# Performance work log

Hardware: AMD Instinct MI355X
Metric: run time of the kernel (lower is better)

Reference implementation:

```python
import jax, jax.numpy as jnp
import numpy as np

# geomloss SamplesLoss defaults: loss='sinkhorn', p=2, blur=0.05, scaling=0.5,
# reach=None (balanced -> dampening lambda = 1), diameter=3, debias=False.
P = 2
DIAMETER = 3.0
BLUR = 0.05
SCALING = 0.5
MARGIN = 0.1
GAMMA = 10.0
# geomloss epsilon_schedule(p, diameter, blur, scaling)
EPS_LIST = [DIAMETER ** P] \
    + [float(np.exp(e)) for e in np.arange(P * np.log(DIAMETER), P * np.log(BLUR), P * np.log(SCALING))] \
    + [BLUR ** P]
NEG_INF_LOGW = -100000.0  # geomloss log_weights() sentinel for zero weights


def similarity_cost(xa, xb, gamma=GAMMA):
    # F.normalize(x, dim=-1): x / max(||x||, 1e-12)
    xa = xa / jnp.clip(jnp.linalg.norm(xa, axis=-1, keepdims=True), 1e-12)
    xb = xb / jnp.clip(jnp.linalg.norm(xb, axis=-1, keepdims=True), 1e-12)
    sim = jnp.exp(jnp.einsum('bnd,bmd->bnm', xa, xb) * gamma)  # (B, N, M)
    sim_c = sim.sum(axis=1, keepdims=True)  # column sums (B, 1, M)
    sim_r = sim.sum(axis=2, keepdims=True)  # row sums    (B, N, 1)
    return 1.0 - sim / (sim_c + sim_r - sim)


def softmin(eps, C, h):
    # geomloss softmin_tensorized: -eps * logsumexp_j(h_j - C_ij/eps)
    # C: (B, N, M), h: (B_or_1, M) -> (B, N)
    return -eps * jax.nn.logsumexp(h[:, None, :] - C / eps, axis=2)


def sinkhorn_ot(alpha, a_log, beta, b_log, f1, f2):
    # geomloss sinkhorn_tensorized with debias=False, balanced OT.
    C_xy = similarity_cost(f1, jax.lax.stop_gradient(f2))  # cost(x, y.detach())
    C_yx = similarity_cost(f2, jax.lax.stop_gradient(f1))  # cost(y, x.detach())
    C_xy_sg = jax.lax.stop_gradient(C_xy)
    C_yx_sg = jax.lax.stop_gradient(C_yx)

    eps = EPS_LIST[0]
    g_ab = softmin(eps, C_yx_sg, a_log)  # dual potential on y
    f_ba = softmin(eps, C_xy_sg, b_log)  # dual potential on x
    for eps in EPS_LIST:
        # symmetric (averaged) Sinkhorn updates, no grad (geomloss runs under no_grad)
        ft = softmin(eps, C_xy_sg, b_log + g_ab / eps)
        gt = softmin(eps, C_yx_sg, a_log + f_ba / eps)
        f_ba, g_ab = 0.5 * (f_ba + ft), 0.5 * (g_ab + gt)

    # last extrapolation: only differentiable step (detached dual inputs)
    eps = EPS_LIST[-1]
    f_ba_new = softmin(eps, C_xy, jax.lax.stop_gradient(b_log + g_ab / eps))
    g_ab_new = softmin(eps, C_yx, jax.lax.stop_gradient(a_log + f_ba / eps))

    # sinkhorn_cost (debias=False): <alpha, f_ba> + <beta, g_ab>
    return (alpha * f_ba_new).sum(axis=1) + (beta * g_ab_new).sum(axis=1)  # (B,)


def setup_inputs() -> dict:
    key = jax.random.key(0)
    k1, k2, k3, k4, k5 = jax.random.split(key, 5)
    B, N, N1, M1, D = 16, 512, 384, 384, 256
    return {
        'x1': jax.random.normal(k1, (B, N, D), dtype=jnp.float32),
        'x2': jax.random.normal(k2, (B, N, D), dtype=jnp.float32),
        'x3': jax.random.normal(k3, (B, N1, D), dtype=jnp.float32),
        'x4': jax.random.normal(k4, (B, M1, D), dtype=jnp.float32),
        'dist': jax.random.normal(k5, (16,), dtype=jnp.float32),  # stored but unused
    }


def reference(x1, x2, x3, x4, dist):
    B, N, _ = x1.shape
    N1 = x3.shape[1]
    M1 = x4.shape[1]
    dt = x1.dtype
    # marginals: ones over real points, zeros over padding points
    alpha = jnp.concatenate([jnp.ones((1, N), dt), jnp.zeros((1, N1), dt)], axis=1)
    beta = jnp.concatenate([jnp.ones((1, N), dt), jnp.zeros((1, M1), dt)], axis=1)
    a_log = jnp.concatenate([jnp.zeros((1, N), dt), jnp.full((1, N1), NEG_INF_LOGW, dt)], axis=1)
    b_log = jnp.concatenate([jnp.zeros((1, N), dt), jnp.full((1, M1), NEG_INF_LOGW, dt)], axis=1)

    f1 = jnp.concatenate([x1, x3], axis=1)  # (B, N+N1, D)
    f2 = jnp.concatenate([x2, x4], axis=1)  # (B, N+M1, D)

    ot_loss = sinkhorn_ot(alpha, a_log, beta, b_log, f1, f2)  # (B,)
    scon_cost = jnp.mean(ot_loss)[None]  # sum(ot_loss)/B, shape (1,)

    hinge = jax.nn.relu(MARGIN - jnp.einsum('bnd,bmd->bnm', x3, x4)).sum()
    hinge_cost = hinge[None]  # shape (1,)

    # original returns {'hinge_cost': ..., 'scon_cost': ...}; pack as (2,) array
    return jnp.concatenate([hinge_cost, scon_cost])
```

## Files before the change

### kernel.cpp

```cpp
#include <hip/hip_runtime.h>
#include <cstddef>
#include <cstdint>

#define BATCH 16
#define NFULL 896
#define NREAL 512
#define NPAD  384
#define DIM   256

typedef short bf16x8 __attribute__((ext_vector_type(8)));
typedef short s16x4  __attribute__((ext_vector_type(4)));
typedef float f32x4  __attribute__((ext_vector_type(4)));
typedef int   int4v  __attribute__((ext_vector_type(4)));

static __device__ inline short f2bf(float v) {
    unsigned u = __float_as_uint(v);
    unsigned r = (u + 0x7FFFu + ((u >> 16) & 1u)) >> 16;
    return (short)r;
}
static __device__ inline float bf2f(short s) {
    return __uint_as_float(((unsigned)(unsigned short)s) << 16);
}

__global__ __launch_bounds__(256) void norm_cvt_kernel(
    const float* __restrict__ x1, const float* __restrict__ x3,
    const float* __restrict__ x2, const float* __restrict__ x4,
    short* __restrict__ A1s, short* __restrict__ B2s,
    float* __restrict__ invn1, float* __restrict__ invn2,
    float* __restrict__ n1, float* __restrict__ n2,
    float* __restrict__ zero_base, float* __restrict__ out)
{
    const int t = threadIdx.x;
    const int gid = blockIdx.x * 256 + t;
    if (gid < 2 * BATCH * NFULL) zero_base[gid] = 0.f;
    if (gid < 2) out[gid] = 0.f;

    const int w = t >> 6, lane = t & 63;
    const int rg = blockIdx.x * 4 + w;
    const int side = rg >= BATCH * NFULL;
    const int rem  = rg - (side ? BATCH * NFULL : 0);
    const int b = rem / NFULL, row = rem % NFULL;
    const float* src;
    if (!side) src = (row < NREAL) ? x1 + ((size_t)b * NREAL + row) * DIM
                                   : x3 + ((size_t)b * NPAD + (row - NREAL)) * DIM;
    else       src = (row < NREAL) ? x2 + ((size_t)b * NREAL + row) * DIM
                                   : x4 + ((size_t)b * NPAD + (row - NREAL)) * DIM;
    const f32x4 v = ((const f32x4*)src)[lane];
    float ss = v[0]*v[0] + v[1]*v[1] + v[2]*v[2] + v[3]*v[3];
    #pragma unroll
    for (int m = 1; m < 64; m <<= 1) ss += __shfl_xor(ss, m);
    const float nrm = sqrtf(ss);
    const float inv = 1.0f / fmaxf(nrm, 1e-12f);
    if (lane == 0) {
        (side ? invn2 : invn1)[b * NFULL + row] = inv;
        (side ? n2 : n1)[b * NFULL + row] = nrm;
    }
    s16x4 hi, lo;
    #pragma unroll
    for (int c = 0; c < 4; ++c) {
        const float val = v[c] * inv;
        hi[c] = f2bf(val);
        lo[c] = f2bf(val - bf2f(hi[c]));
    }
    short* dst = (side ? B2s : A1s) + ((size_t)b * NFULL + row) * 512;
    *(s16x4*)(dst + lane * 4) = hi;
    *(s16x4*)(dst + 256 + lane * 4) = lo;
}

__global__ __launch_bounds__(256) void gram_mfma_kernel(
    const short* __restrict__ A1s, const short* __restrict__ B2s,
    const float* __restrict__ n1, const float* __restrict__ n2,
    float* __restrict__ S, float* __restrict__ rowsum, float* __restrict__ colsum,
    float* __restrict__ out_hinge)
{
    const int flat = blockIdx.x;
    const int id = (flat & 7) * 98 + (flat >> 3);
    const int b  = id / 49;
    const int r49 = id % 49;
    const int by = r49 / 7, bx = r49 % 7;
    const int i0 = by * 128;
    const int j0 = bx * 128;
    __shared__ __align__(16) short As[128][72];
    __shared__ __align__(16) short Bs[128][72];
    const int t = threadIdx.x;
    const int wid = t >> 6, lane = t & 63;
    const int wr = wid >> 1, wc = wid & 1;
    const int lr = lane & 15, lg = lane >> 4;
    f32x4 acc[4][4] = {};

    const short* gA = A1s + ((size_t)b * NFULL + i0) * 512;
    const short* gB = B2s + ((size_t)b * NFULL + j0) * 512;

    for (int step = 0; step < 12; ++step) {
        const int kb   = step * 64;
        const int koff = kb & 255;
        const int aoff = (((kb >> 8) == 1) ? 256 : 0) + koff;
        const int boff = (((kb >> 8) == 2) ? 256 : 0) + koff;
        __syncthreads();
        #pragma unroll
        for (int p = 0; p < 4; ++p) {
            const int s = p * 256 + t;
            const int row = s >> 3, c = s & 7;
            *(int4v*)((char*)&As[0][0] + row * 144 + c * 16) =
                *(const int4v*)(gA + (size_t)row * 512 + aoff + c * 8);
            *(int4v*)((char*)&Bs[0][0] + row * 144 + c * 16) =
                *(const int4v*)(gB + (size_t)row * 512 + boff + c * 8);
        }
        __syncthreads();
        #pragma unroll
        for (int kk = 0; kk < 64; kk += 32) {
            bf16x8 af[4], bg[4];
            #pragma unroll
            for (int m = 0; m < 4; ++m)
                af[m] = *(const bf16x8*)((const char*)&As[0][0]
                         + (wr * 64 + m * 16 + lr) * 144 + kk * 2 + lg * 16);
            #pragma unroll
            for (int n = 0; n < 4; ++n)
                bg[n] = *(const bf16x8*)((const char*)&Bs[0][0]
                         + (wc * 64 + n * 16 + lr) * 144 + kk * 2 + lg * 16);
            #pragma unroll
            for (int m = 0; m < 4; ++m)
                #pragma unroll
                for (int n = 0; n < 4; ++n)
                    acc[m][n] = __builtin_amdgcn_mfma_f32_16x16x32_bf16(
                        af[m], bg[n], acc[m][n], 0, 0, 0);
        }
    }

    const bool storeS = (by < 4) && (bx < 4);
    const bool hingeB = (by >= 4) && (bx >= 4);
    float rp[4][4] = {};
    float cp[4] = {};
    float hp = 0.f;
    #pragma unroll
    for (int m = 0; m < 4; ++m) {
        const int row0 = i0 + wr * 64 + m * 16 + lg * 4;
        float n1v[4] = {0.f, 0.f, 0.f, 0.f};
        if (hingeB) {
            #pragma unroll
            for (int r = 0; r < 4; ++r) n1v[r] = n1[b * NFULL + row0 + r];
        }
        #pragma unroll
        for (int n = 0; n < 4; ++n) {
            const int col = j0 + wc * 64 + n * 16 + lr;
            const f32x4 f = acc[m][n];
            float cn = 0.f;
            float sv[4];
            #pragma unroll
            for (int r = 0; r < 4; ++r) {
                sv[r] = __expf(10.f * f[r]);
                rp[m][r] += sv[r];
                cn += sv[r];
            }
            cp[n] += cn;
            if (storeS) {
                #pragma unroll
                for (int r = 0; r < 4; ++r)
                    S[((size_t)b * NREAL + row0 + r) * NREAL + col] = sv[r];
            }
            if (hingeB) {
                const float nn2 = n2[b * NFULL + col];
                #pragma unroll
                for (int r = 0; r < 4; ++r)
                    hp += fmaxf(0.1f - f[r] * n1v[r] * nn2, 0.f);
            }
        }
    }
    #pragma unroll
    for (int m = 0; m < 4; ++m)
        #pragma unroll
        for (int r = 0; r < 4; ++r) {
            float v = rp[m][r];
            v += __shfl_xor(v, 1); v += __shfl_xor(v, 2);
            v += __shfl_xor(v, 4); v += __shfl_xor(v, 8);
            if (lr == 0)
                atomicAdd(&rowsum[b * NFULL + i0 + wr * 64 + m * 16 + lg * 4 + r], v);
        }
    #pragma unroll
    for (int n = 0; n < 4; ++n) {
        float v = cp[n];
        v += __shfl_xor(v, 16); v += __shfl_xor(v, 32);
        if (lg == 0)
            atomicAdd(&colsum[b * NFULL + j0 + wc * 64 + n * 16 + lr], v);
    }
    if (hingeB) {
        #pragma unroll
        for (int m = 1; m < 64; m <<= 1) hp += __shfl_xor(hp, m);
        if (lane == 0) atomicAdd(out_hinge, hp);
    }
}

__global__ __launch_bounds__(256) void norm_kernel(
    const float* __restrict__ x1, const float* __restrict__ x3,
    const float* __restrict__ x2, const float* __restrict__ x4,
    float* __restrict__ invn1, float* __restrict__ invn2)
{
    const int w = threadIdx.x >> 6, lane = threadIdx.x & 63;
    const int rg = blockIdx.x * 4 + w;
    const int side = rg / (BATCH * NFULL);
    const int rem  = rg - side * (BATCH * NFULL);
    const int b = rem / NFULL, r = rem % NFULL;
    const float* src;
    if (side == 0)
        src = (r < NREAL) ? x1 + ((size_t)b * NREAL + r) * DIM
                          : x3 + ((size_t)b * NPAD + (r - NREAL)) * DIM;
    else
        src = (r < NREAL) ? x2 + ((size_t)b * NREAL + r) * DIM
                          : x4 + ((size_t)b * NPAD + (r - NREAL)) * DIM;
    float4 v = ((const float4*)src)[lane];
    float ss = v.x*v.x + v.y*v.y + v.z*v.z + v.w*v.w;
    #pragma unroll
    for (int m = 1; m < 64; m <<= 1) ss += __shfl_xor(ss, m);
    if (lane == 0)
        (side == 0 ? invn1 : invn2)[b * NFULL + r] = 1.0f / fmaxf(sqrtf(ss), 1e-12f);
}

__global__ __launch_bounds__(256) void gram_kernel(
    const float* __restrict__ x1, const float* __restrict__ x3,
    const float* __restrict__ x2, const float* __restrict__ x4,
    const float* __restrict__ invn1, const float* __restrict__ invn2,
    float* __restrict__ S, float* __restrict__ rowsum, float* __restrict__ colsum)
{
    const int b  = blockIdx.z;
    const int i0 = blockIdx.y * 64;
    const int j0 = blockIdx.x * 64;
    __shared__ float As[64][68];
    __shared__ float Bs[64][68];
    __shared__ float rsh[64], csh[64];
    const int t = threadIdx.x;
    const int tx = t & 15, ty = t >> 4;
    if (t < 64) { rsh[t] = 0.f; csh[t] = 0.f; }
    float acc[4][4] = {};
    const int lk = t & 63, r4 = t >> 6;
    for (int kc = 0; kc < DIM; kc += 64) {
        __syncthreads();
        #pragma unroll
        for (int rr = 0; rr < 64; rr += 4) {
            const int r = rr + r4;
            const int gi = i0 + r;
            const float* pa = (gi < NREAL) ? x1 + ((size_t)b * NREAL + gi) * DIM
                                           : x3 + ((size_t)b * NPAD + (gi - NREAL)) * DIM;
            As[r][lk] = pa[kc + lk] * invn1[b * NFULL + gi];
            const int gj = j0 + r;
            const float* pb = (gj < NREAL) ? x2 + ((size_t)b * NREAL + gj) * DIM
                                           : x4 + ((size_t)b * NPAD + (gj - NREAL)) * DIM;
            Bs[r][lk] = pb[kc + lk] * invn2[b * NFULL + gj];
        }
        __syncthreads();
        #pragma unroll
        for (int k = 0; k < 64; k += 4) {
            float4 av[4], bv[4];
            #pragma unroll
            for (int u = 0; u < 4; ++u) av[u] = *(const float4*)&As[ty + 16*u][k];
            #pragma unroll
            for (int u = 0; u < 4; ++u) bv[u] = *(const float4*)&Bs[tx + 16*u][k];
            #pragma unroll
            for (int u = 0; u < 4; ++u)
                #pragma unroll
                for (int v = 0; v < 4; ++v) {
                    acc[u][v] += av[u].x * bv[v].x;
                    acc[u][v] += av[u].y * bv[v].y;
                    acc[u][v] += av[u].z * bv[v].z;
                    acc[u][v] += av[u].w * bv[v].w;
                }
        }
    }
    float rpart[4] = {}, cpart[4] = {};
    const bool store = (i0 < NREAL) && (j0 < NREAL);
    #pragma unroll
    for (int u = 0; u < 4; ++u)
        #pragma unroll
        for (int v = 0; v < 4; ++v) {
            const float s = __expf(10.0f * acc[u][v]);
            rpart[u] += s;
            cpart[v] += s;
            if (store) {
                const int i = i0 + ty + 16*u, j = j0 + tx + 16*v;
                S[((size_t)b * NREAL + i) * NREAL + j] = s;
            }
        }
    #pragma unroll
    for (int u = 0; u < 4; ++u) atomicAdd(&rsh[ty + 16*u], rpart[u]);
    #pragma unroll
    for (int v = 0; v < 4; ++v) atomicAdd(&csh[tx + 16*v], cpart[v]);
    __syncthreads();
    if (t < 64) {
        atomicAdd(&rowsum[b * NFULL + i0 + t], rsh[t]);
        atomicAdd(&colsum[b * NFULL + j0 + t], csh[t]);
    }
}

__global__ __launch_bounds__(256) void hinge_kernel(
    const float* __restrict__ x3, const float* __restrict__ x4, float* __restrict__ out)
{
    const int b  = blockIdx.z;
    const int i0 = blockIdx.y * 64;
    const int j0 = blockIdx.x * 64;
    __shared__ float As[64][68];
    __shared__ float Bs[64][68];
    const int t = threadIdx.x;
    const int tx = t & 15, ty = t >> 4;
    float acc[4][4] = {};
    const int lk = t & 63, r4 = t >> 6;
    for (int kc = 0; kc < DIM; kc += 64) {
        __syncthreads();
        #pragma unroll
        for (int rr = 0; rr < 64; rr += 4) {
            const int r = rr + r4;
            As[r][lk] = x3[((size_t)b * NPAD + i0 + r) * DIM + kc + lk];
            Bs[r][lk] = x4[((size_t)b * NPAD + j0 + r) * DIM + kc + lk];
        }
        __syncthreads();
        #pragma unroll
        for (int k = 0; k < 64; k += 4) {
            float4 av[4], bv[4];
            #pragma unroll
            for (int u = 0; u < 4; ++u) av[u] = *(const float4*)&As[ty + 16*u][k];
            #pragma unroll
            for (int u = 0; u < 4; ++u) bv[u] = *(const float4*)&Bs[tx + 16*u][k];
            #pragma unroll
            for (int u = 0; u < 4; ++u)
                #pragma unroll
                for (int v = 0; v < 4; ++v) {
                    acc[u][v] += av[u].x * bv[v].x;
                    acc[u][v] += av[u].y * bv[v].y;
                    acc[u][v] += av[u].z * bv[v].z;
                    acc[u][v] += av[u].w * bv[v].w;
                }
        }
    }
    float part = 0.f;
    #pragma unroll
    for (int u = 0; u < 4; ++u)
        #pragma unroll
        for (int v = 0; v < 4; ++v) part += fmaxf(0.1f - acc[u][v], 0.f);
    __shared__ float red[256];
    red[t] = part;
    __syncthreads();
    for (int s = 128; s > 0; s >>= 1) { if (t < s) red[t] += red[t + s]; __syncthreads(); }
    if (t == 0) atomicAdd(out, red[0]);
}

__global__ __launch_bounds__(256) void cost_kernel(
    float* __restrict__ C, float* __restrict__ CT,
    const float* __restrict__ rowsum, const float* __restrict__ colsum)
{
    const int b  = blockIdx.z;
    const int i0 = blockIdx.y * 64, j0 = blockIdx.x * 64;
    __shared__ float tile[64][65];
    const int t = threadIdx.x;
    const int lj = t & 63, r4 = t >> 6;
    #pragma unroll
    for (int rr = 0; rr < 64; rr += 4) {
        const int li = rr + r4;
        const size_t idx = ((size_t)b * NREAL + i0 + li) * NREAL + j0 + lj;
        const float s  = C[idx];
        const float rs = rowsum[b * NFULL + i0 + li];
        const float cs = colsum[b * NFULL + j0 + lj];
        const float c = 1.0f - s / (rs + cs - s);
        C[idx] = c;
        tile[li][lj] = c;
    }
    if (CT == nullptr) return;
    __syncthreads();
    #pragma unroll
    for (int rr = 0; rr < 4 * 16; rr += 4) {
        const int lc = rr + r4;
        CT[((size_t)b * NREAL + j0 + lc) * NREAL + i0 + lj] = tile[lj][lc];
    }
}

__global__ __launch_bounds__(256) void softmin_kernel(
    const float* __restrict__ C, const float* __restrict__ CT,
    const float* __restrict__ f_in, const float* __restrict__ g_in,
    float* __restrict__ f_out, float* __restrict__ g_out,
    float eps, int mode, float* __restrict__ out)
{
    const int w = threadIdx.x >> 6, lane = threadIdx.x & 63;
    const int rg = blockIdx.x * 4 + w;
    const int side = rg >= 2048;
    const int rem  = side ? rg - 2048 : rg;
    const int b  = rem >> 7;
    const int ib = (rem & 127) * 4;
    const float inv_eps = 1.0f / eps;
    const float* h_src = (side ? f_in : g_in) + b * NREAL;

    f32x4 h0 = {0.f, 0.f, 0.f, 0.f}, h1 = h0;
    if (mode != 0) {
        const f32x4* h4 = (const f32x4*)h_src;
        h0 = h4[lane] * inv_eps;
        h1 = h4[64 + lane] * inv_eps;
    }

    const float* Mb;
    size_t stride;
    if (!side)   { Mb = C  + ((size_t)(b * NREAL + ib)) * NREAL; stride = 1; }
    else if (CT) { Mb = CT + ((size_t)(b * NREAL + ib)) * NREAL; stride = 1; }
    else         { Mb = C + (size_t)b * NREAL * NREAL + ib;      stride = NREAL; }

    float res[4];
    float acc_res = 0.f;
    if (stride == 1) {
        f32x4 A0[4], A1[4];
        #pragma unroll
        for (int rr = 0; rr < 4; ++rr) {
            const f32x4* M4 = (const f32x4*)(Mb + (size_t)rr * NREAL);
            A0[rr] = M4[lane];
            A1[rr] = M4[64 + lane];
        }
        #pragma unroll
        for (int rr = 0; rr < 4; ++rr) {
            const f32x4 v0 = h0 - A0[rr] * inv_eps;
            const f32x4 v1 = h1 - A1[rr] * inv_eps;
            float mx = fmaxf(fmaxf(fmaxf(v0[0], v0[1]), fmaxf(v0[2], v0[3])),
                             fmaxf(fmaxf(v1[0], v1[1]), fmaxf(v1[2], v1[3])));
            #pragma unroll
            for (int off = 1; off < 64; off <<= 1) mx = fmaxf(mx, __shfl_xor(mx, off));
            float s = 0.f;
            #pragma unroll
            for (int c = 0; c < 4; ++c) s += __expf(v0[c] - mx);
            #pragma unroll
            for (int c = 0; c < 4; ++c) s += __expf(v1[c] - mx);
            #pragma unroll
            for (int off = 1; off < 64; off <<= 1) s += __shfl_xor(s, off);
            res[rr] = -eps * (mx + __logf(s));
            acc_res += res[rr];
        }
    } else {
        #pragma unroll
        for (int rr = 0; rr < 4; ++rr) {
            const float* M = Mb + rr;
            float v[8];
            #pragma unroll
            for (int q = 0; q < 8; ++q) {
                const float h = (q < 4) ? h0[q & 3] : h1[q & 3];
                v[q] = h - M[(size_t)((q & 3) + (q >> 2) * 256 + lane * 4) * NREAL
                             - (size_t)(lane * 4 + (q & 3) + (q >> 2) * 256) * 0] * inv_eps;
            }
            #pragma unroll
            for (int q = 0; q < 8; ++q) {
                const int j = (q >> 2) * 256 + lane * 4 + (q & 3);
                v[q] = ((q < 4) ? h0[q & 3] : h1[q & 3]) - M[(size_t)j * NREAL] * inv_eps;
            }
            float mx = v[0];
            #pragma unroll
            for (int q = 1; q < 8; ++q) mx = fmaxf(mx, v[q]);
            #pragma unroll
            for (int off = 1; off < 64; off <<= 1) mx = fmaxf(mx, __shfl_xor(mx, off));
            float s = 0.f;
            #pragma unroll
            for (int q = 0; q < 8; ++q) s += __expf(v[q] - mx);
            #pragma unroll
            for (int off = 1; off < 64; off <<= 1) s += __shfl_xor(s, off);
            res[rr] = -eps * (mx + __logf(s));
            acc_res += res[rr];
        }
    }

    if (mode == 2) {
        __shared__ float sred[4];
        if (lane == 0) sred[w] = acc_res;
        __syncthreads();
        if (threadIdx.x == 0)
            atomicAdd(out, (sred[0] + sred[1] + sred[2] + sred[3]) * (1.0f / BATCH));
    } else if (lane == 0) {
        float* st = (side ? g_out : f_out) + b * NREAL + ib;
        if (mode == 0) {
            *(f32x4*)st = f32x4{res[0], res[1], res[2], res[3]};
        } else {
            const f32x4 si = *(const f32x4*)((side ? g_in : f_in) + b * NREAL + ib);
            *(f32x4*)st = 0.5f * (si + f32x4{res[0], res[1], res[2], res[3]});
        }
    }
}

extern "C" void kernel_launch(void* const* d_in, const int* in_sizes, int n_in,
                              void* d_out, int out_size, void* d_ws, size_t ws_size,
                              hipStream_t stream)
{
    const float* x1 = (const float*)d_in[0];
    const float* x2 = (const float*)d_in[1];
    const float* x3 = (const float*)d_in[2];
    const float* x4 = (const float*)d_in[3];
    float* out = (float*)d_out;

    char* p = (char*)d_ws;
    const size_t CBYTES = (size_t)BATCH * NREAL * NREAL * 4;
    const size_t ABYTES = (size_t)BATCH * NFULL * 512 * 2;
    const size_t NB = (size_t)BATCH * NFULL * 4;
    const size_t PB = (size_t)BATCH * NREAL * 4;
    const size_t SMALLB = 6 * NB + 4 * PB;
    const bool mfma_ok = ws_size >= CBYTES + 2 * ABYTES + SMALLB;

    float* C = (float*)p; p += CBYTES;
    short* A1s = nullptr; short* B2s = nullptr;
    float* CT = nullptr;
    if (mfma_ok) {
        A1s = (short*)p; p += ABYTES;
        B2s = (short*)p; p += ABYTES;
        CT = (float*)A1s;
    }
    float* rowsum = (float*)p; p += NB;
    float* colsum = (float*)p; p += NB;
    float* invn1  = (float*)p; p += NB;
    float* invn2  = (float*)p; p += NB;
    float* n1     = (float*)p; p += NB;
    float* n2     = (float*)p; p += NB;
    float* fs     = (float*)p; p += 2 * PB;
    float* gs     = (float*)p; p += 2 * PB;
    if (!mfma_ok && ws_size >= (size_t)(p - (char*)d_ws) + CBYTES) {
        CT = (float*)p; p += CBYTES;
    }
    const int PS = BATCH * NREAL;

    if (mfma_ok) {
        norm_cvt_kernel<<<(2 * BATCH * NFULL) / 4, 256, 0, stream>>>(
            x1, x3, x2, x4, A1s, B2s, invn1, invn2, n1, n2, rowsum, out);
        gram_mfma_kernel<<<784, 256, 0, stream>>>(
            A1s, B2s, n1, n2, C, rowsum, colsum, out);
    } else {
        hipMemsetAsync(out, 0, 2 * sizeof(float), stream);
        hipMemsetAsync(rowsum, 0, 2 * NB, stream);
        norm_kernel<<<(2 * BATCH * NFULL) / 4, 256, 0, stream>>>(
            x1, x3, x2, x4, invn1, invn2);
        gram_kernel<<<dim3(14, 14, BATCH), 256, 0, stream>>>(
            x1, x3, x2, x4, invn1, invn2, C, rowsum, colsum);
        hinge_kernel<<<dim3(6, 6, BATCH), 256, 0, stream>>>(x3, x4, out);
    }
    cost_kernel<<<dim3(8, 8, BATCH), 256, 0, stream>>>(C, CT, rowsum, colsum);

    const int SMB = 1024;
    const float epsl[8] = {9.0f, 9.0f, 2.25f, 0.5625f, 0.140625f,
                           0.03515625f, 0.0087890625f, 0.0025f};

    softmin_kernel<<<SMB, 256, 0, stream>>>(C, CT, fs, gs, fs, gs, 9.0f, 0, out);
    int cur = 0;
    for (int k = 0; k < 8; ++k) {
        softmin_kernel<<<SMB, 256, 0, stream>>>(C, CT,
            fs + cur * PS, gs + cur * PS,
            fs + (1 - cur) * PS, gs + (1 - cur) * PS,
            epsl[k], 1, out);
        cur ^= 1;
    }
    softmin_kernel<<<SMB, 256, 0, stream>>>(C, CT,
        fs + cur * PS, gs + cur * PS, nullptr, nullptr,
        0.0025f, 2, out + 1);
}
```

Before: 200.8 us.

## Fuse cost and Sinkhorn iterations into one cooperative kernel; use direct-to-LDS swizzled loads

Replaces the cost kernel plus ten separate softmin launches with one cooperative persistent kernel that uses grid.sync between iterations, removing per-launch overhead and inter-kernel gaps. The gram MFMA kernel now loads tiles with global_load_lds into XOR-swizzled unpadded LDS instead of going through registers. It also skips row/column sum atomics for padding tiles and remaps softmin work so each XCD handles whole batches. The cooperative path adds grid barrier costs and depends on occupancy queries and host attribute calls made on every launch.

```diff
diff --git a/kernel.cpp b/kernel.cpp
--- a/kernel.cpp
+++ b/kernel.cpp
@@ -1,6 +1,9 @@
 #include <hip/hip_runtime.h>
+#include <hip/hip_cooperative_groups.h>
 #include <cstddef>
 #include <cstdint>
+
+namespace cg = cooperative_groups;
 
 #define BATCH 16
 #define NFULL 896
@@ -11,7 +14,6 @@
 typedef short bf16x8 __attribute__((ext_vector_type(8)));
 typedef short s16x4  __attribute__((ext_vector_type(4)));
 typedef float f32x4  __attribute__((ext_vector_type(4)));
-typedef int   int4v  __attribute__((ext_vector_type(4)));
 
 static __device__ inline short f2bf(float v) {
     unsigned u = __float_as_uint(v);
@@ -20,6 +22,15 @@
 }
 static __device__ inline float bf2f(short s) {
     return __uint_as_float(((unsigned)(unsigned short)s) << 16);
+}
+
+static __device__ __forceinline__ void gload_lds16(const void* g, size_t lds_byte_off,
+                                                   void* lds_base) {
+    __builtin_amdgcn_global_load_lds(
+        (const __attribute__((address_space(1))) unsigned int*)(size_t)g,
+        (__attribute__((address_space(3))) unsigned int*)(unsigned int)
+            ((size_t)lds_base + lds_byte_off),
+        16, 0, 0);
 }
 
 __global__ __launch_bounds__(256) void norm_cvt_kernel(
@@ -80,8 +91,8 @@
     const int by = r49 / 7, bx = r49 % 7;
     const int i0 = by * 128;
     const int j0 = bx * 128;
-    __shared__ __align__(16) short As[128][72];
-    __shared__ __align__(16) short Bs[128][72];
+    __shared__ __align__(16) short As[128][64];
+    __shared__ __align__(16) short Bs[128][64];
     const int t = threadIdx.x;
     const int wid = t >> 6, lane = t & 63;
     const int wr = wid >> 1, wc = wid & 1;
@@ -91,6 +102,14 @@
     const short* gA = A1s + ((size_t)b * NFULL + i0) * 512;
     const short* gB = B2s + ((size_t)b * NFULL + j0) * 512;
 
+    int srow[4], scl[4];
+    #pragma unroll
+    for (int p = 0; p < 4; ++p) {
+        const int s = p * 256 + t;
+        srow[p] = s >> 3;
+        scl[p] = (s & 7) ^ (srow[p] & 7);
+    }
+
     for (int step = 0; step < 12; ++step) {
         const int kb   = step * 64;
         const int koff = kb & 255;
@@ -98,26 +117,29 @@
         const int boff = (((kb >> 8) == 2) ? 256 : 0) + koff;
         __syncthreads();
         #pragma unroll
-        for (int p = 0; p < 4; ++p) {
-            const int s = p * 256 + t;
-            const int row = s >> 3, c = s & 7;
-            *(int4v*)((char*)&As[0][0] + row * 144 + c * 16) =
-                *(const int4v*)(gA + (size_t)row * 512 + aoff + c * 8);
-            *(int4v*)((char*)&Bs[0][0] + row * 144 + c * 16) =
-                *(const int4v*)(gB + (size_t)row * 512 + boff + c * 8);
-        }
-        __syncthreads();
-        #pragma unroll
-        for (int kk = 0; kk < 64; kk += 32) {
+        for (int p = 0; p < 4; ++p)
+            gload_lds16(gA + (size_t)srow[p] * 512 + aoff + scl[p] * 8,
+                        (size_t)(p * 256 + wid * 64) * 16, &As[0][0]);
+        #pragma unroll
+        for (int p = 0; p < 4; ++p)
+            gload_lds16(gB + (size_t)srow[p] * 512 + boff + scl[p] * 8,
+                        (size_t)(p * 256 + wid * 64) * 16, &Bs[0][0]);
+        __syncthreads();
+        #pragma unroll
+        for (int kk = 0; kk < 2; ++kk) {
             bf16x8 af[4], bg[4];
             #pragma unroll
-            for (int m = 0; m < 4; ++m)
+            for (int m = 0; m < 4; ++m) {
+                const int row = wr * 64 + m * 16 + lr;
                 af[m] = *(const bf16x8*)((const char*)&As[0][0]
-                         + (wr * 64 + m * 16 + lr) * 144 + kk * 2 + lg * 16);
-            #pragma unroll
-            for (int n = 0; n < 4; ++n)
+                         + row * 128 + (((kk * 4 + lg) ^ (row & 7)) << 4));
+            }
+            #pragma unroll
+            for (int n = 0; n < 4; ++n) {
+                const int row = wc * 64 + n * 16 + lr;
                 bg[n] = *(const bf16x8*)((const char*)&Bs[0][0]
-                         + (wc * 64 + n * 16 + lr) * 144 + kk * 2 + lg * 16);
+                         + row * 128 + (((kk * 4 + lg) ^ (row & 7)) << 4));
+            }
             #pragma unroll
             for (int m = 0; m < 4; ++m)
                 #pragma unroll
@@ -166,27 +188,265 @@
             }
         }
     }
-    #pragma unroll
-    for (int m = 0; m < 4; ++m)
-        #pragma unroll
-        for (int r = 0; r < 4; ++r) {
-            float v = rp[m][r];
-            v += __shfl_xor(v, 1); v += __shfl_xor(v, 2);
-            v += __shfl_xor(v, 4); v += __shfl_xor(v, 8);
-            if (lr == 0)
-                atomicAdd(&rowsum[b * NFULL + i0 + wr * 64 + m * 16 + lg * 4 + r], v);
-        }
-    #pragma unroll
-    for (int n = 0; n < 4; ++n) {
-        float v = cp[n];
-        v += __shfl_xor(v, 16); v += __shfl_xor(v, 32);
-        if (lg == 0)
-            atomicAdd(&colsum[b * NFULL + j0 + wc * 64 + n * 16 + lr], v);
+    if (by < 4) {
+        #pragma unroll
+        for (int m = 0; m < 4; ++m)
+            #pragma unroll
+            for (int r = 0; r < 4; ++r) {
+                float v = rp[m][r];
+                v += __shfl_xor(v, 1); v += __shfl_xor(v, 2);
+                v += __shfl_xor(v, 4); v += __shfl_xor(v, 8);
+                if (lr == 0)
+                    atomicAdd(&rowsum[b * NFULL + i0 + wr * 64 + m * 16 + lg * 4 + r], v);
+            }
+    }
+    if (bx < 4) {
+        #pragma unroll
+        for (int n = 0; n < 4; ++n) {
+            float v = cp[n];
+            v += __shfl_xor(v, 16); v += __shfl_xor(v, 32);
+            if (lg == 0)
+                atomicAdd(&colsum[b * NFULL + j0 + wc * 64 + n * 16 + lr], v);
+        }
     }
     if (hingeB) {
         #pragma unroll
         for (int m = 1; m < 64; m <<= 1) hp += __shfl_xor(hp, m);
         if (lane == 0) atomicAdd(out_hinge, hp);
+    }
+}
+
+static __device__ __forceinline__ void softmin_task(
+    int vb, int w, int lane,
+    const float* __restrict__ C, const float* __restrict__ CT,
+    const float* __restrict__ fin, const float* __restrict__ gin,
+    float* __restrict__ fout, float* __restrict__ gout,
+    float eps, int mode, float* __restrict__ out, float* sred)
+{
+    const int xcd = vb & 7;
+    const int wv  = (vb >> 3) * 4 + w;
+    const int side = wv >> 8;
+    const int b  = 2 * xcd + ((wv >> 7) & 1);
+    const int ib = (wv & 127) * 4;
+    const float inv_eps = 1.0f / eps;
+
+    f32x4 h0 = {0.f, 0.f, 0.f, 0.f}, h1 = h0;
+    if (mode != 0) {
+        const f32x4* h4 = (const f32x4*)((side ? fin : gin) + b * NREAL);
+        h0 = h4[lane] * inv_eps;
+        h1 = h4[64 + lane] * inv_eps;
+    }
+    const float* Mb = (side ? CT : C) + ((size_t)(b * NREAL + ib)) * NREAL;
+    f32x4 A0[4], A1[4];
+    #pragma unroll
+    for (int rr = 0; rr < 4; ++rr) {
+        const f32x4* M4 = (const f32x4*)(Mb + (size_t)rr * NREAL);
+        A0[rr] = M4[lane];
+        A1[rr] = M4[64 + lane];
+    }
+    float res[4];
+    float accr = 0.f;
+    #pragma unroll
+    for (int rr = 0; rr < 4; ++rr) {
+        const f32x4 v0 = h0 - A0[rr] * inv_eps;
+        const f32x4 v1 = h1 - A1[rr] * inv_eps;
+        float mx = fmaxf(fmaxf(fmaxf(v0[0], v0[1]), fmaxf(v0[2], v0[3])),
+                         fmaxf(fmaxf(v1[0], v1[1]), fmaxf(v1[2], v1[3])));
+        #pragma unroll
+        for (int off = 1; off < 64; off <<= 1) mx = fmaxf(mx, __shfl_xor(mx, off));
+        float s = 0.f;
+        #pragma unroll
+        for (int c = 0; c < 4; ++c) s += __expf(v0[c] - mx);
+        #pragma unroll
+        for (int c = 0; c < 4; ++c) s += __expf(v1[c] - mx);
+        #pragma unroll
+        for (int off = 1; off < 64; off <<= 1) s += __shfl_xor(s, off);
+        res[rr] = -eps * (mx + __logf(s));
+        accr += res[rr];
+    }
+    if (mode == 2) {
+        if (lane == 0) sred[w] = accr;
+        __syncthreads();
+        if (w == 0 && lane == 0)
+            atomicAdd(out, (sred[0] + sred[1] + sred[2] + sred[3]) * (1.0f / BATCH));
+        __syncthreads();
+    } else if (lane == 0) {
+        float* st = (side ? gout : fout) + b * NREAL + ib;
+        if (mode == 0) {
+            *(f32x4*)st = f32x4{res[0], res[1], res[2], res[3]};
+        } else {
+            const f32x4 si = *(const f32x4*)((side ? gin : fin) + b * NREAL + ib);
+            *(f32x4*)st = 0.5f * (si + f32x4{res[0], res[1], res[2], res[3]});
+        }
+    }
+}
+
+__global__ __launch_bounds__(256, 4) void sinkhorn_coop_kernel(
+    float* __restrict__ C, float* __restrict__ CT,
+    const float* __restrict__ rowsum, const float* __restrict__ colsum,
+    float* __restrict__ fs, float* __restrict__ gs, float* __restrict__ out)
+{
+    cg::grid_group grid = cg::this_grid();
+    const int t = threadIdx.x;
+    const int w = t >> 6, lane = t & 63;
+    __shared__ float tile[64][65];
+    __shared__ float sred[4];
+
+    for (int vb = blockIdx.x; vb < 1024; vb += gridDim.x) {
+        const int xcd = vb & 7;
+        const int t128 = vb >> 3;
+        const int b = 2 * xcd + (t128 >> 6);
+        const int t64 = t128 & 63;
+        const int i0 = (t64 >> 3) * 64, j0 = (t64 & 7) * 64;
+        const int lj = t & 63, r4 = t >> 6;
+        __syncthreads();
+        #pragma unroll
+        for (int rr = 0; rr < 64; rr += 4) {
+            const int li = rr + r4;
+            const size_t idx = ((size_t)(b * NREAL + i0 + li)) * NREAL + j0 + lj;
+            const float s  = C[idx];
+            const float c = 1.0f - s / (rowsum[b * NFULL + i0 + li]
+                                        + colsum[b * NFULL + j0 + lj] - s);
+            C[idx] = c;
+            tile[li][lj] = c;
+        }
+        __syncthreads();
+        #pragma unroll
+        for (int rr = 0; rr < 64; rr += 4) {
+            const int lc = rr + r4;
+            CT[((size_t)(b * NREAL + j0 + lc)) * NREAL + i0 + lj] = tile[lj][lc];
+        }
+    }
+    grid.sync();
+
+    const float epsl[8] = {9.0f, 9.0f, 2.25f, 0.5625f, 0.140625f,
+                           0.03515625f, 0.0087890625f, 0.0025f};
+    float* f0 = fs;            float* g0 = gs;
+    float* f1 = fs + BATCH * NREAL;
+    float* g1 = gs + BATCH * NREAL;
+
+    for (int vb = blockIdx.x; vb < 1024; vb += gridDim.x)
+        softmin_task(vb, w, lane, C, CT, nullptr, nullptr, f0, g0, 9.0f, 0,
+                     nullptr, sred);
+    grid.sync();
+
+    float* fc = f0; float* gc = g0; float* fa = f1; float* ga = g1;
+    #pragma unroll
+    for (int k = 0; k < 8; ++k) {
+        for (int vb = blockIdx.x; vb < 1024; vb += gridDim.x)
+            softmin_task(vb, w, lane, C, CT, fc, gc, fa, ga, epsl[k], 1,
+                         nullptr, sred);
+        grid.sync();
+        float* tf = fc; fc = fa; fa = tf;
+        float* tg = gc; gc = ga; ga = tg;
+    }
+
+    for (int vb = blockIdx.x; vb < 1024; vb += gridDim.x)
+        softmin_task(vb, w, lane, C, CT, fc, gc, nullptr, nullptr, 0.0025f, 2,
+                     out + 1, sred);
+}
+
+__global__ __launch_bounds__(256) void cost_kernel(
+    float* __restrict__ C, float* __restrict__ CT,
+    const float* __restrict__ rowsum, const float* __restrict__ colsum)
+{
+    const int b  = blockIdx.z;
+    const int i0 = blockIdx.y * 64, j0 = blockIdx.x * 64;
+    __shared__ float tile[64][65];
+    const int t = threadIdx.x;
+    const int lj = t & 63, r4 = t >> 6;
+    #pragma unroll
+    for (int rr = 0; rr < 64; rr += 4) {
+        const int li = rr + r4;
+        const size_t idx = ((size_t)b * NREAL + i0 + li) * NREAL + j0 + lj;
+        const float s  = C[idx];
+        const float c = 1.0f - s / (rowsum[b * NFULL + i0 + li]
+                                    + colsum[b * NFULL + j0 + lj] - s);
+        C[idx] = c;
+        tile[li][lj] = c;
+    }
+    if (CT == nullptr) return;
+    __syncthreads();
+    #pragma unroll
+    for (int rr = 0; rr < 64; rr += 4) {
+        const int lc = rr + r4;
+        CT[((size_t)b * NREAL + j0 + lc) * NREAL + i0 + lj] = tile[lj][lc];
+    }
+}
+
+__global__ __launch_bounds__(256) void softmin_kernel(
+    const float* __restrict__ C, const float* __restrict__ CT,
+    const float* __restrict__ f_in, const float* __restrict__ g_in,
+    float* __restrict__ f_out, float* __restrict__ g_out,
+    float eps, int mode, float* __restrict__ out)
+{
+    const int w = threadIdx.x >> 6, lane = threadIdx.x & 63;
+    const int rg = blockIdx.x * 4 + w;
+    const int side = rg >= 2048;
+    const int rem  = side ? rg - 2048 : rg;
+    const int b  = rem >> 7;
+    const int ib = (rem & 127) * 4;
+    const float inv_eps = 1.0f / eps;
+    const float* h_src = (side ? f_in : g_in) + b * NREAL;
+
+    f32x4 h0 = {0.f, 0.f, 0.f, 0.f}, h1 = h0;
+    if (mode != 0) {
+        const f32x4* h4 = (const f32x4*)h_src;
+        h0 = h4[lane] * inv_eps;
+        h1 = h4[64 + lane] * inv_eps;
+    }
+    const float* Mb;
+    size_t stride;
+    if (!side)   { Mb = C  + ((size_t)(b * NREAL + ib)) * NREAL; stride = 1; }
+    else if (CT) { Mb = CT + ((size_t)(b * NREAL + ib)) * NREAL; stride = 1; }
+    else         { Mb = C + (size_t)b * NREAL * NREAL + ib;      stride = NREAL; }
+
+    float res[4];
+    float acc_res = 0.f;
+    #pragma unroll
+    for (int rr = 0; rr < 4; ++rr) {
+        float v[8];
+        if (stride == 1) {
+            const f32x4* M4 = (const f32x4*)(Mb + (size_t)rr * NREAL);
+            const f32x4 a0 = M4[lane], a1 = M4[64 + lane];
+            #pragma unroll
+            for (int c = 0; c < 4; ++c) { v[c] = h0[c] - a0[c] * inv_eps;
+                                          v[4+c] = h1[c] - a1[c] * inv_eps; }
+        } else {
+            const float* M = Mb + rr;
+            #pragma unroll
+            for (int q = 0; q < 8; ++q) {
+                const int j = (q >> 2) * 256 + lane * 4 + (q & 3);
+                v[q] = ((q < 4) ? h0[q & 3] : h1[q & 3]) - M[(size_t)j * NREAL] * inv_eps;
+            }
+        }
+        float mx = v[0];
+        #pragma unroll
+        for (int q = 1; q < 8; ++q) mx = fmaxf(mx, v[q]);
+        #pragma unroll
+        for (int off = 1; off < 64; off <<= 1) mx = fmaxf(mx, __shfl_xor(mx, off));
+        float s = 0.f;
+        #pragma unroll
+        for (int q = 0; q < 8; ++q) s += __expf(v[q] - mx);
+        #pragma unroll
+        for (int off = 1; off < 64; off <<= 1) s += __shfl_xor(s, off);
+        res[rr] = -eps * (mx + __logf(s));
+        acc_res += res[rr];
+    }
+    if (mode == 2) {
+        __shared__ float sred[4];
+        if (lane == 0) sred[w] = acc_res;
+        __syncthreads();
+        if (threadIdx.x == 0)
+            atomicAdd(out, (sred[0] + sred[1] + sred[2] + sred[3]) * (1.0f / BATCH));
+    } else if (lane == 0) {
+        float* st = (side ? g_out : f_out) + b * NREAL + ib;
+        if (mode == 0) {
+            *(f32x4*)st = f32x4{res[0], res[1], res[2], res[3]};
+        } else {
+            const f32x4 si = *(const f32x4*)((side ? g_in : f_in) + b * NREAL + ib);
+            *(f32x4*)st = 0.5f * (si + f32x4{res[0], res[1], res[2], res[3]});
+        }
     }
 }
 
@@ -341,139 +601,6 @@
     if (t == 0) atomicAdd(out, red[0]);
 }
 
-__global__ __launch_bounds__(256) void cost_kernel(
-    float* __restrict__ C, float* __restrict__ CT,
-    const float* __restrict__ rowsum, const float* __restrict__ colsum)
-{
-    const int b  = blockIdx.z;
-    const int i0 = blockIdx.y * 64, j0 = blockIdx.x * 64;
-    __shared__ float tile[64][65];
-    const int t = threadIdx.x;
-    const int lj = t & 63, r4 = t >> 6;
-    #pragma unroll
-    for (int rr = 0; rr < 64; rr += 4) {
-        const int li = rr + r4;
-        const size_t idx = ((size_t)b * NREAL + i0 + li) * NREAL + j0 + lj;
-        const float s  = C[idx];
-        const float rs = rowsum[b * NFULL + i0 + li];
-        const float cs = colsum[b * NFULL + j0 + lj];
-        const float c = 1.0f - s / (rs + cs - s);
-        C[idx] = c;
-        tile[li][lj] = c;
-    }
-    if (CT == nullptr) return;
-    __syncthreads();
-    #pragma unroll
-    for (int rr = 0; rr < 4 * 16; rr += 4) {
-        const int lc = rr + r4;
-        CT[((size_t)b * NREAL + j0 + lc) * NREAL + i0 + lj] = tile[lj][lc];
-    }
-}
-
-__global__ __launch_bounds__(256) void softmin_kernel(
-    const float* __restrict__ C, const float* __restrict__ CT,
-    const float* __restrict__ f_in, const float* __restrict__ g_in,
-    float* __restrict__ f_out, float* __restrict__ g_out,
-    float eps, int mode, float* __restrict__ out)
-{
-    const int w = threadIdx.x >> 6, lane = threadIdx.x & 63;
-    const int rg = blockIdx.x * 4 + w;
-    const int side = rg >= 2048;
-    const int rem  = side ? rg - 2048 : rg;
-    const int b  = rem >> 7;
-    const int ib = (rem & 127) * 4;
-    const float inv_eps = 1.0f / eps;
-    const float* h_src = (side ? f_in : g_in) + b * NREAL;
-
-    f32x4 h0 = {0.f, 0.f, 0.f, 0.f}, h1 = h0;
-    if (mode != 0) {
-        const f32x4* h4 = (const f32x4*)h_src;
-        h0 = h4[lane] * inv_eps;
-        h1 = h4[64 + lane] * inv_eps;
-    }
-
-    const float* Mb;
-    size_t stride;
-    if (!side)   { Mb = C  + ((size_t)(b * NREAL + ib)) * NREAL; stride = 1; }
-    else if (CT) { Mb = CT + ((size_t)(b * NREAL + ib)) * NREAL; stride = 1; }
-    else         { Mb = C + (size_t)b * NREAL * NREAL + ib;      stride = NREAL; }
-
-    float res[4];
-    float acc_res = 0.f;
-    if (stride == 1) {
-        f32x4 A0[4], A1[4];
-        #pragma unroll
-        for (int rr = 0; rr < 4; ++rr) {
-            const f32x4* M4 = (const f32x4*)(Mb + (size_t)rr * NREAL);
-            A0[rr] = M4[lane];
-            A1[rr] = M4[64 + lane];
-        }
-        #pragma unroll
-        for (int rr = 0; rr < 4; ++rr) {
-            const f32x4 v0 = h0 - A0[rr] * inv_eps;
-            const f32x4 v1 = h1 - A1[rr] * inv_eps;
-            float mx = fmaxf(fmaxf(fmaxf(v0[0], v0[1]), fmaxf(v0[2], v0[3])),
-                             fmaxf(fmaxf(v1[0], v1[1]), fmaxf(v1[2], v1[3])));
-            #pragma unroll
-            for (int off = 1; off < 64; off <<= 1) mx = fmaxf(mx, __shfl_xor(mx, off));
-            float s = 0.f;
-            #pragma unroll
-            for (int c = 0; c < 4; ++c) s += __expf(v0[c] - mx);
-            #pragma unroll
-            for (int c = 0; c < 4; ++c) s += __expf(v1[c] - mx);
-            #pragma unroll
-            for (int off = 1; off < 64; off <<= 1) s += __shfl_xor(s, off);
-            res[rr] = -eps * (mx + __logf(s));
-            acc_res += res[rr];
-        }
-    } else {
-        #pragma unroll
-        for (int rr = 0; rr < 4; ++rr) {
-            const float* M = Mb + rr;
-            float v[8];
-            #pragma unroll
-            for (int q = 0; q < 8; ++q) {
-                const float h = (q < 4) ? h0[q & 3] : h1[q & 3];
-                v[q] = h - M[(size_t)((q & 3) + (q >> 2) * 256 + lane * 4) * NREAL
-                             - (size_t)(lane * 4 + (q & 3) + (q >> 2) * 256) * 0] * inv_eps;
-            }
-            #pragma unroll
-            for (int q = 0; q < 8; ++q) {
-                const int j = (q >> 2) * 256 + lane * 4 + (q & 3);
-                v[q] = ((q < 4) ? h0[q & 3] : h1[q & 3]) - M[(size_t)j * NREAL] * inv_eps;
-            }
-            float mx = v[0];
-            #pragma unroll
-            for (int q = 1; q < 8; ++q) mx = fmaxf(mx, v[q]);
-            #pragma unroll
-            for (int off = 1; off < 64; off <<= 1) mx = fmaxf(mx, __shfl_xor(mx, off));
-            float s = 0.f;
-            #pragma unroll
-            for (int q = 0; q < 8; ++q) s += __expf(v[q] - mx);
-            #pragma unroll
-            for (int off = 1; off < 64; off <<= 1) s += __shfl_xor(s, off);
-            res[rr] = -eps * (mx + __logf(s));
-            acc_res += res[rr];
-        }
-    }
-
-    if (mode == 2) {
-        __shared__ float sred[4];
-        if (lane == 0) sred[w] = acc_res;
-        __syncthreads();
-        if (threadIdx.x == 0)
-            atomicAdd(out, (sred[0] + sred[1] + sred[2] + sred[3]) * (1.0f / BATCH));
-    } else if (lane == 0) {
-        float* st = (side ? g_out : f_out) + b * NREAL + ib;
-        if (mode == 0) {
-            *(f32x4*)st = f32x4{res[0], res[1], res[2], res[3]};
-        } else {
-            const f32x4 si = *(const f32x4*)((side ? g_in : f_in) + b * NREAL + ib);
-            *(f32x4*)st = 0.5f * (si + f32x4{res[0], res[1], res[2], res[3]});
-        }
-    }
-}
-
 extern "C" void kernel_launch(void* const* d_in, const int* in_sizes, int n_in,
                               void* d_out, int out_size, void* d_ws, size_t ws_size,
                               hipStream_t stream)
@@ -512,6 +639,19 @@
         CT = (float*)p; p += CBYTES;
     }
     const int PS = BATCH * NREAL;
+
+    int dev = 0;
+    hipGetDevice(&dev);
+    int coopAttr = 0;
+    hipDeviceGetAttribute(&coopAttr, hipDeviceAttributeCooperativeLaunch, dev);
+    int numCU = 0;
+    hipDeviceGetAttribute(&numCU, hipDeviceAttributeMultiprocessorCount, dev);
+    int maxB = 0;
+    hipOccupancyMaxActiveBlocksPerMultiprocessor(
+        &maxB, (const void*)sinkhorn_coop_kernel, 256, 0);
+    int coopGrid = maxB * numCU;
+    if (coopGrid > 1024) coopGrid = 1024;
+    const bool use_coop = mfma_ok && coopAttr && coopGrid >= 8;
 
     if (mfma_ok) {
         norm_cvt_kernel<<<(2 * BATCH * NFULL) / 4, 256, 0, stream>>>(
@@ -527,12 +667,18 @@
             x1, x3, x2, x4, invn1, invn2, C, rowsum, colsum);
         hinge_kernel<<<dim3(6, 6, BATCH), 256, 0, stream>>>(x3, x4, out);
     }
+
+    if (use_coop) {
+        void* args[] = {&C, &CT, &rowsum, &colsum, &fs, &gs, &out};
+        hipLaunchCooperativeKernel((void*)sinkhorn_coop_kernel,
+                                   dim3(coopGrid), dim3(256), args, 0, stream);
+        return;
+    }
+
     cost_kernel<<<dim3(8, 8, BATCH), 256, 0, stream>>>(C, CT, rowsum, colsum);
-
     const int SMB = 1024;
     const float epsl[8] = {9.0f, 9.0f, 2.25f, 0.5625f, 0.140625f,
                            0.03515625f, 0.0087890625f, 0.0025f};
-
     softmin_kernel<<<SMB, 256, 0, stream>>>(C, CT, fs, gs, fs, gs, 9.0f, 0, out);
     int cur = 0;
     for (int k = 0; k < 8; ++k) {
```

Measured after the change: 656.0 us. +226.7%, slower.
